# Optimization experiments

Hardware: AMD Instinct MI355X
Metric: run time of the kernel (lower is better)

Reference implementation:

```python
import math
import jax, jax.numpy as jnp
import numpy as np

N_LAYER = 4
D = 256            # n_embd
NH = 4             # n_head
MLP_MULT = 128
VOCAB = 256
N = D * MLP_MULT // NH   # 8192 neurons per head
LN_EPS = 1e-5
TWO_PI = 2.0 * math.pi


def get_freqs(n, theta=2.0 ** 16):
    # quantize(arange(n), q=2) = floor(t/2)*2
    t = jnp.floor(jnp.arange(n, dtype=jnp.float32) / 2.0) * 2.0
    return 1.0 / theta ** (t / n) / TWO_PI


def layernorm(x):
    # nn.LayerNorm(D, elementwise_affine=False): plain normalization
    m = jnp.mean(x, axis=-1, keepdims=True)
    v = jnp.var(x, axis=-1, keepdims=True)
    return (x - m) / jnp.sqrt(v + LN_EPS)


def rope(phases, v):
    # v_rot interleaves (-v_odd, v_even) pairs
    v_rot = jnp.stack((-v[..., 1::2], v[..., ::2]), axis=-1).reshape(v.shape)
    p = (phases % 1.0) * TWO_PI
    return v * jnp.cos(p) + v_rot * jnp.sin(p)


def attention(x_sparse, x):
    # Q = K = x_sparse: (B, nh, T, N); V = x: (B, 1, T, D)
    T = x_sparse.shape[2]
    freqs = get_freqs(N).reshape(1, 1, 1, N)
    phases = jnp.arange(T, dtype=jnp.float32).reshape(1, 1, T, 1) * freqs
    QR = rope(phases, x_sparse)                       # (B, nh, T, N)
    scores = jnp.einsum('bhtn,bhsn->bhts', QR, QR)    # (B, nh, T, T)
    mask = jnp.tril(jnp.ones((T, T), dtype=bool), k=-1)  # strict lower tri
    scores = jnp.where(mask, scores, 0.0)
    return scores @ x                                 # (B, nh, T, D), V broadcast over heads


def bdh_forward(idx, embed, encoder, encoder_v, decoder, lm_head):
    B, T = idx.shape
    x = embed[idx][:, None]        # (B, 1, T, D)
    x = layernorm(x)
    dec = decoder.reshape(NH, N, D)
    for _ in range(N_LAYER):
        x_latent = jnp.einsum('btd,hdn->bhtn', x[:, 0], encoder)   # D -> N expand
        x_sparse = jax.nn.relu(x_latent)
        yKV = attention(x_sparse, x)                               # (B, nh, T, D)
        yKV = layernorm(yKV)
        y_latent = jnp.einsum('bhtd,hdn->bhtn', yKV, encoder_v)
        y_sparse = jax.nn.relu(y_latent)
        xy_sparse = x_sparse * y_sparse                            # gate
        yMLP = jnp.einsum('bhtn,hnd->btd', xy_sparse, dec)         # N -> D decode
        x = layernorm(x + yMLP[:, None])                           # residual + LN
    logits = x[:, 0] @ lm_head    # (B, T, vocab)
    return logits


def setup_inputs() -> dict:
    key = jax.random.key(0)
    k1, k2, k3, k4, k5, k6 = jax.random.split(key, 6)
    B, T = 2, 512
    std = 0.02
    return {
        'idx': jax.random.randint(k1, (B, T), 0, VOCAB, dtype=jnp.int64 if jax.config.jax_enable_x64 else jnp.int32),
        'embed': jax.random.normal(k2, (VOCAB, D), dtype=jnp.float32) * std,
        'encoder': jax.random.normal(k3, (NH, D, N), dtype=jnp.float32) * std,
        'encoder_v': jax.random.normal(k4, (NH, D, N), dtype=jnp.float32) * std,
        'decoder': jax.random.normal(k5, (NH * N, D), dtype=jnp.float32) * std,
        'lm_head': jax.random.normal(k6, (D, VOCAB), dtype=jnp.float32) * std,
    }


def reference(idx, embed, encoder, encoder_v, decoder, lm_head):
    return bdh_forward(idx, embed, encoder, encoder_v, decoder, lm_head)
```

## Files before the change

kernel.cpp:

```cpp
#include <hip/hip_runtime.h>
#include <hip/hip_bf16.h>
#include <cstdio>

#define DEV static __device__ __forceinline__

typedef __attribute__((ext_vector_type(4))) float floatx4;
typedef __attribute__((ext_vector_type(8))) __bf16 bf16x8;

constexpr int Bv = 2, Tv = 512, Dv = 256, NHv = 4, Nv = 8192, NLv = 4, Vv = 256;
constexpr int BTv = Bv * Tv;
constexpr int BHv = Bv * NHv;
constexpr float LNEPS = 1e-5f;
constexpr int KS_SC = 8;
constexpr int KS_DEC = 8;

DEV float b2f(short s) {
    unsigned u = ((unsigned)(unsigned short)s) << 16;
    return __builtin_bit_cast(float, u);
}
DEV short f2b(float f) {
    unsigned u = __builtin_bit_cast(unsigned, f);
    u = (u + 0x7fffu + ((u >> 16) & 1u)) >> 16;
    return (short)u;
}

typedef __attribute__((address_space(3))) unsigned int lds_u32;
typedef const __attribute__((address_space(1))) unsigned int glb_u32;
DEV void gload16(const short* g, short* ldsbase) {
    __builtin_amdgcn_global_load_lds((glb_u32*)g, (lds_u32*)ldsbase, 16, 0, 0);
}

__global__ __launch_bounds__(256) void k_cvtT(const float* __restrict__ in,
                                              short* __restrict__ out, int R, int C) {
    __shared__ float tile[32][33];
    const float* ib = in + (size_t)blockIdx.z * R * C;
    short* ob = out + (size_t)blockIdx.z * R * C;
    int c0 = blockIdx.x * 32, r0 = blockIdx.y * 32;
    int tx = threadIdx.x & 31, ty = threadIdx.x >> 5;
#pragma unroll
    for (int i = 0; i < 4; i++) {
        int r = r0 + ty + i * 8;
        tile[ty + i * 8][tx] = ib[(size_t)r * C + c0 + tx];
    }
    __syncthreads();
#pragma unroll
    for (int i = 0; i < 4; i++) {
        int c = c0 + ty + i * 8;
        ob[(size_t)c * R + r0 + tx] = f2b(tile[tx][ty + i * 8]);
    }
}

__global__ __launch_bounds__(256) void k_transp(const short* __restrict__ xb,
                                                short* __restrict__ xbT) {
    __shared__ short tile[32][33];
    int b = blockIdx.z;
    int t0 = blockIdx.x * 32, d0 = blockIdx.y * 32;
    int tx = threadIdx.x & 31, ty = threadIdx.x >> 5;
#pragma unroll
    for (int i = 0; i < 4; i++)
        tile[ty + i * 8][tx] = xb[((size_t)b * Tv + t0 + ty + i * 8) * Dv + d0 + tx];
    __syncthreads();
#pragma unroll
    for (int i = 0; i < 4; i++)
        xbT[((size_t)b * Dv + d0 + ty + i * 8) * Tv + t0 + tx] = tile[tx][ty + i * 8];
}

__global__ __launch_bounds__(256) void k_rope(unsigned* __restrict__ tab) {
    int i = blockIdx.x * 256 + threadIdx.x;
    int t = blockIdx.y;
    float f = exp2f(-(float)i / 256.0f) * 0.15915494309189535f;
    float ph = fmodf((float)t * f, 1.0f) * 6.2831853071795864f;
    unsigned c = (unsigned short)f2b(cosf(ph));
    unsigned s = (unsigned short)f2b(sinf(ph));
    tab[(size_t)t * (Nv / 2) + i] = c | (s << 16);
}

DEV void reduce2(float& s1, float& s2) {
    __shared__ float r1[4];
    __shared__ float r2[4];
#pragma unroll
    for (int o = 32; o > 0; o >>= 1) {
        s1 += __shfl_down(s1, o, 64);
        s2 += __shfl_down(s2, o, 64);
    }
    int lane = threadIdx.x & 63, w = threadIdx.x >> 6;
    if (lane == 0) { r1[w] = s1; r2[w] = s2; }
    __syncthreads();
    s1 = r1[0] + r1[1] + r1[2] + r1[3];
    s2 = r2[0] + r2[1] + r2[2] + r2[3];
}

DEV float ln_val(float v, float s1, float s2) {
    float m = s1 * (1.0f / Dv);
    float var = s2 * (1.0f / Dv) - m * m;
    float inv = rsqrtf(var + LNEPS);
    return (v - m) * inv;
}

__global__ __launch_bounds__(256) void k_embed_ln(const int* __restrict__ idx,
                                                  const float* __restrict__ embed,
                                                  float* __restrict__ xf, short* __restrict__ xb) {
    int r = blockIdx.x, d = threadIdx.x;
    float v = embed[(size_t)idx[r] * Dv + d];
    float s1 = v, s2 = v * v;
    reduce2(s1, s2);
    float o = ln_val(v, s1, s2);
    xf[(size_t)r * Dv + d] = o;
    xb[(size_t)r * Dv + d] = f2b(o);
}

__global__ __launch_bounds__(256) void k_ln(const float* __restrict__ in,
                                            short* __restrict__ outb) {
    int r = blockIdx.x, d = threadIdx.x;
    size_t o = (size_t)r * Dv + d;
    float v = in[o];
    float s1 = v, s2 = v * v;
    reduce2(s1, s2);
    outb[o] = f2b(ln_val(v, s1, s2));
}

__global__ __launch_bounds__(256) void k_lnsum(const short* __restrict__ ymb,
                                               float* __restrict__ xf, short* __restrict__ xb) {
    int r = blockIdx.x, d = threadIdx.x;
    size_t o = (size_t)r * Dv + d;
    float v = xf[o];
#pragma unroll
    for (int z = 0; z < NHv * KS_DEC; z++)
        v += b2f(ymb[(size_t)z * BTv * Dv + o]);
    float s1 = v, s2 = v * v;
    reduce2(s1, s2);
    float res = ln_val(v, s1, s2);
    xf[o] = res;
    xb[o] = f2b(res);
}

DEV void gemm_main(const short* __restrict__ Ab, int lda,
                   const short* __restrict__ Bb, int ldb, int K,
                   short* sA, short* sB, floatx4 acc[4][4]) {
    const int tid = threadIdx.x;
    const int lane = tid & 63, w = tid >> 6;
    const int wr = w >> 1, wc = w & 1;
    const int lrow = lane & 15;
    const int q = lane >> 4;
    const int rsw = (lrow >> 1) & 3;
    const int srow = lane >> 2;
    const int ssw = (lane & 3) ^ ((lane >> 3) & 3);
    for (int kk = 0; kk < K; kk += 32) {
        __syncthreads();
#pragma unroll
        for (int g2 = 0; g2 < 2; g2++) {
            int brow = g2 * 64 + w * 16;
            int grow = brow + srow;
            gload16(&Ab[(size_t)grow * lda + kk + ssw * 8], &sA[brow * 32]);
            gload16(&Bb[(size_t)grow * ldb + kk + ssw * 8], &sB[brow * 32]);
        }
        __syncthreads();
        bf16x8 aF[4], bF[4];
#pragma unroll
        for (int m = 0; m < 4; m++)
            aF[m] = *(const bf16x8*)&sA[(wr * 64 + m * 16 + lrow) * 32 + ((q ^ rsw) * 8)];
#pragma unroll
        for (int n = 0; n < 4; n++)
            bF[n] = *(const bf16x8*)&sB[(wc * 64 + n * 16 + lrow) * 32 + ((q ^ rsw) * 8)];
#pragma unroll
        for (int m = 0; m < 4; m++)
#pragma unroll
            for (int n = 0; n < 4; n++)
                acc[m][n] = __builtin_amdgcn_mfma_f32_16x16x32_bf16(aF[m], bF[n], acc[m][n], 0, 0, 0);
    }
}

__global__ __launch_bounds__(256) void k_latent(const short* __restrict__ xb,
                                                const short* __restrict__ encT,
                                                const unsigned* __restrict__ ropeT,
                                                short* __restrict__ qr) {
    __shared__ short sA[128 * 32];
    __shared__ short sB[128 * 32];
    int bid = blockIdx.x;
    int xcd = bid & 7, rr = bid >> 3;
    int cmb = xcd + 8 * (rr & 31);
    int mb = rr >> 5;
    int nb = cmb & 63, h = cmb >> 6;
    const short* Ab = xb + (size_t)mb * 128 * Dv;
    const short* Bb = encT + (size_t)h * Nv * Dv + (size_t)nb * 128 * Dv;
    floatx4 acc[4][4] = {};
    gemm_main(Ab, Dv, Bb, Dv, Dv, sA, sB, acc);
    int lane = threadIdx.x & 63, w = threadIdx.x >> 6, wr = w >> 1, wc = w & 1;
    int rb = (lane >> 4) * 4, cb = lane & 15;
    float sgn = (cb & 1) ? 1.0f : -1.0f;
#pragma unroll
    for (int m = 0; m < 4; m++)
#pragma unroll
        for (int n = 0; n < 4; n++) {
            int col = nb * 128 + wc * 64 + n * 16 + cb;
#pragma unroll
            for (int r = 0; r < 4; r++) {
                int row = mb * 128 + wr * 64 + m * 16 + rb + r;
                int b = row >> 9, t = row & 511;
                float v = acc[m][n][r];
                v = v > 0.f ? v : 0.f;
                float vp = __shfl_xor(v, 1);
                unsigned cs = ropeT[(size_t)t * (Nv / 2) + (col >> 1)];
                float c = b2f((short)(cs & 0xffff)), s = b2f((short)(cs >> 16));
                qr[((size_t)(b * NHv + h) * Tv + t) * Nv + col] = f2b(v * c + sgn * vp * s);
            }
        }
}

__global__ __launch_bounds__(256) void k_scores(const short* __restrict__ qr,
                                                short* __restrict__ scs) {
    __shared__ short sA[128 * 32];
    __shared__ short sB[128 * 32];
    int bid = blockIdx.x;
    int xcd = bid & 7, rr = bid >> 3;
    int cmb = xcd + 8 * (rr & 7);
    int pb = rr >> 3;
    int bh = cmb & 7, ks = cmb >> 3;
    int tb = 0;
    while (((tb + 1) * (tb + 2)) / 2 <= pb) tb++;
    int sb = pb - (tb * (tb + 1)) / 2;
    const bool diag = (tb == sb);
    const int KC = Nv / KS_SC;
    const short* Ab = qr + ((size_t)bh * Tv + tb * 128) * Nv + ks * KC;
    const short* Bb = qr + ((size_t)bh * Tv + sb * 128) * Nv + ks * KC;
    floatx4 acc[4][4] = {};
    const int tid = threadIdx.x, lane = tid & 63, w = tid >> 6;
    const int wr = w >> 1, wc = w & 1;
    const int lrow = lane & 15;
    const int q = lane >> 4;
    const int rsw = (lrow >> 1) & 3;
    const int srow = lane >> 2;
    const int ssw = (lane & 3) ^ ((lane >> 3) & 3);
    for (int kk = 0; kk < KC; kk += 32) {
        __syncthreads();
#pragma unroll
        for (int g2 = 0; g2 < 2; g2++) {
            int brow = g2 * 64 + w * 16;
            int grow = brow + srow;
            gload16(&Ab[(size_t)grow * Nv + kk + ssw * 8], &sA[brow * 32]);
            if (!diag)
                gload16(&Bb[(size_t)grow * Nv + kk + ssw * 8], &sB[brow * 32]);
        }
        __syncthreads();
        const short* sBr = diag ? sA : sB;
        bf16x8 aF[4], bF[4];
#pragma unroll
        for (int m = 0; m < 4; m++)
            aF[m] = *(const bf16x8*)&sA[(wr * 64 + m * 16 + lrow) * 32 + ((q ^ rsw) * 8)];
#pragma unroll
        for (int n = 0; n < 4; n++)
            bF[n] = *(const bf16x8*)&sBr[(wc * 64 + n * 16 + lrow) * 32 + ((q ^ rsw) * 8)];
#pragma unroll
        for (int m = 0; m < 4; m++)
#pragma unroll
            for (int n = 0; n < 4; n++)
                acc[m][n] = __builtin_amdgcn_mfma_f32_16x16x32_bf16(aF[m], bF[n], acc[m][n], 0, 0, 0);
    }
    short* slab = scs + ((size_t)ks * BHv + bh) * Tv * Tv;
    int rb = (lane >> 4) * 4, cb = lane & 15;
#pragma unroll
    for (int m = 0; m < 4; m++)
#pragma unroll
        for (int n = 0; n < 4; n++)
#pragma unroll
            for (int r = 0; r < 4; r++) {
                int t = tb * 128 + wr * 64 + m * 16 + rb + r;
                int s = sb * 128 + wc * 64 + n * 16 + cb;
                slab[(size_t)t * Tv + s] = f2b(acc[m][n][r]);
            }
}

__global__ __launch_bounds__(256) void k_redsc(const short* __restrict__ scs,
                                               short* __restrict__ scb) {
    int c = blockIdx.x * 256 + threadIdx.x;
    int row = c >> 6;
    int s0 = (c & 63) * 8;
    int t = row & (Tv - 1);
    float a[8] = {};
#pragma unroll
    for (int ks = 0; ks < KS_SC; ks++) {
        int4 raw = *(const int4*)&scs[((size_t)ks * BHv * Tv + row) * Tv + s0];
        const short* rs = (const short*)&raw;
#pragma unroll
        for (int j = 0; j < 8; j++) a[j] += b2f(rs[j]);
    }
    union { short s[8]; int4 v; } u;
#pragma unroll
    for (int j = 0; j < 8; j++) u.s[j] = (s0 + j < t) ? f2b(a[j]) : 0;
    *(int4*)&scb[(size_t)row * Tv + s0] = u.v;
}

__global__ __launch_bounds__(256) void k_pvg(const short* __restrict__ scb,
                                             const short* __restrict__ xbT,
                                             float* __restrict__ ykv) {
    __shared__ short sA[128 * 32];
    __shared__ short sB[128 * 32];
    int mb = blockIdx.x, nb = blockIdx.y, bh = blockIdx.z;
    int b = bh >> 2;
    const short* Ab = scb + ((size_t)bh * Tv + mb * 128) * Tv;
    const short* Bb = xbT + ((size_t)b * Dv + nb * 128) * Tv;
    floatx4 acc[4][4] = {};
    gemm_main(Ab, Tv, Bb, Tv, (mb + 1) * 128, sA, sB, acc);
    int lane = threadIdx.x & 63, w = threadIdx.x >> 6, wr = w >> 1, wc = w & 1;
    int rb = (lane >> 4) * 4, cb = lane & 15;
#pragma unroll
    for (int m = 0; m < 4; m++)
#pragma unroll
        for (int n = 0; n < 4; n++)
#pragma unroll
            for (int r = 0; r < 4; r++) {
                int t = mb * 128 + wr * 64 + m * 16 + rb + r;
                int d = nb * 128 + wc * 64 + n * 16 + cb;
                ykv[((size_t)bh * Tv + t) * Dv + d] = acc[m][n][r];
            }
}

__global__ __launch_bounds__(256) void k_gate(const short* __restrict__ ykvb,
                                              const short* __restrict__ encvT,
                                              const short* __restrict__ qr,
                                              const unsigned* __restrict__ ropeT,
                                              short* __restrict__ xy) {
    __shared__ short sA[128 * 32];
    __shared__ short sB[128 * 32];
    int bid = blockIdx.x;
    int xcd = bid & 7, rr = bid >> 3;
    int cmb = xcd + 8 * (rr & 31);
    int wi = rr >> 5;
    int mb = wi & 3, bq = wi >> 2;
    int nb = cmb & 63, h = cmb >> 6;
    int bh = bq * NHv + h;
    const short* Ab = ykvb + ((size_t)bh * Tv + mb * 128) * Dv;
    const short* Bb = encvT + (size_t)h * Nv * Dv + (size_t)nb * 128 * Dv;
    floatx4 acc[4][4] = {};
    gemm_main(Ab, Dv, Bb, Dv, Dv, sA, sB, acc);
    int lane = threadIdx.x & 63, w = threadIdx.x >> 6, wr = w >> 1, wc = w & 1;
    int rb = (lane >> 4) * 4, cb = lane & 15;
    int par = cb & 1;
    float sgn = par ? 1.0f : -1.0f;
#pragma unroll
    for (int m = 0; m < 4; m++)
#pragma unroll
        for (int n = 0; n < 4; n++) {
            int col = nb * 128 + wc * 64 + n * 16 + cb;
#pragma unroll
            for (int r = 0; r < 4; r++) {
                int t = mb * 128 + wr * 64 + m * 16 + rb + r;
                size_t idx = ((size_t)bh * Tv + t) * Nv + col;
                unsigned pq = *(const unsigned*)&qr[idx & ~(size_t)1];
                float qlo = b2f((short)(pq & 0xffff)), qhi2 = b2f((short)(pq >> 16));
                float qv = par ? qhi2 : qlo;
                float qp = par ? qlo : qhi2;
                unsigned cs = ropeT[(size_t)t * (Nv / 2) + (col >> 1)];
                float c = b2f((short)(cs & 0xffff)), s = b2f((short)(cs >> 16));
                float xsr = qv * c - sgn * qp * s;
                float v = acc[m][n][r];
                v = v > 0.f ? v : 0.f;
                xy[idx] = f2b(v * xsr);
            }
        }
}

__global__ __launch_bounds__(256) void k_decode(const short* __restrict__ xy,
                                                const short* __restrict__ decT,
                                                short* __restrict__ ymb) {
    __shared__ short sA[128 * 32];
    __shared__ short sB[128 * 32];
    int bid = blockIdx.x;
    int xcd = bid & 7, rr = bid >> 3;
    int cmb = xcd + 8 * (rr & 7);
    int mb = rr >> 3;
    int nb = cmb & 1, h = (cmb >> 1) & 3, ks = cmb >> 3;
    const int KC = Nv / KS_DEC;
    int row0 = mb * 128;
    int b = row0 >> 9, t0 = row0 & 511;
    const short* Ab = xy + ((size_t)(b * NHv + h) * Tv + t0) * Nv + ks * KC;
    const short* Bb = decT + (size_t)h * Dv * Nv + (size_t)nb * 128 * Nv + ks * KC;
    floatx4 acc[4][4] = {};
    gemm_main(Ab, Nv, Bb, Nv, KC, sA, sB, acc);
    short* slab = ymb + (size_t)(h * KS_DEC + ks) * BTv * Dv;
    int lane = threadIdx.x & 63, w = threadIdx.x >> 6, wr = w >> 1, wc = w & 1;
    int rb = (lane >> 4) * 4, cb = lane & 15;
#pragma unroll
    for (int m = 0; m < 4; m++)
#pragma unroll
        for (int n = 0; n < 4; n++)
#pragma unroll
            for (int r = 0; r < 4; r++) {
                int row = row0 + wr * 64 + m * 16 + rb + r;
                int col = nb * 128 + wc * 64 + n * 16 + cb;
                slab[(size_t)row * Dv + col] = f2b(acc[m][n][r]);
            }
}

__global__ __launch_bounds__(256) void k_head(const short* __restrict__ xb,
                                              const short* __restrict__ lmhT,
                                              float* __restrict__ out) {
    __shared__ short sA[128 * 32];
    __shared__ short sB[128 * 32];
    int mb = blockIdx.x, nb = blockIdx.y;
    const short* Ab = xb + (size_t)mb * 128 * Dv;
    const short* Bb = lmhT + (size_t)nb * 128 * Dv;
    floatx4 acc[4][4] = {};
    gemm_main(Ab, Dv, Bb, Dv, Dv, sA, sB, acc);
    int lane = threadIdx.x & 63, w = threadIdx.x >> 6, wr = w >> 1, wc = w & 1;
    int rb = (lane >> 4) * 4, cb = lane & 15;
#pragma unroll
    for (int m = 0; m < 4; m++)
#pragma unroll
        for (int n = 0; n < 4; n++)
#pragma unroll
            for (int r = 0; r < 4; r++) {
                int row = mb * 128 + wr * 64 + m * 16 + rb + r;
                int col = nb * 128 + wc * 64 + n * 16 + cb;
                out[(size_t)row * Vv + col] = acc[m][n][r];
            }
}

extern "C" void kernel_launch(void* const* d_in, const int* in_sizes, int n_in,
                              void* d_out, int out_size, void* d_ws, size_t ws_size,
                              hipStream_t stream) {
    const int* idx = (const int*)d_in[0];
    const float* embed = (const float*)d_in[1];
    const float* enc = (const float*)d_in[2];
    const float* encv = (const float*)d_in[3];
    const float* dec = (const float*)d_in[4];
    const float* lmh = (const float*)d_in[5];
    float* out = (float*)d_out;

    char* w = (char*)d_ws;
    size_t off = 0;
    auto alloc = [&](size_t bytes) -> void* {
        void* p = w + off;
        off = (off + bytes + 255) & ~(size_t)255;
        return p;
    };
    short* encT = (short*)alloc((size_t)NHv * Nv * Dv * 2);
    short* encvT = (short*)alloc((size_t)NHv * Nv * Dv * 2);
    short* decT = (short*)alloc((size_t)NHv * Dv * Nv * 2);
    short* lmhT = (short*)alloc((size_t)Vv * Dv * 2);
    unsigned* ropeT = (unsigned*)alloc((size_t)Tv * (Nv / 2) * 4);
    float* xf = (float*)alloc((size_t)BTv * Dv * 4);
    short* xb = (short*)alloc((size_t)BTv * Dv * 2);
    short* xbT = (short*)alloc((size_t)BTv * Dv * 2);
    short* xy = (short*)alloc((size_t)BHv * Tv * Nv * 2);
    short* qr = (short*)alloc((size_t)BHv * Tv * Nv * 2);
    short* scs = (short*)alloc((size_t)KS_SC * BHv * Tv * Tv * 2);
    short* scb = (short*)alloc((size_t)BHv * Tv * Tv * 2);
    float* ykvf = (float*)alloc((size_t)BHv * Tv * Dv * 4);
    short* ykvb = (short*)alloc((size_t)BHv * Tv * Dv * 2);
    short* ymb = (short*)alloc((size_t)NHv * KS_DEC * BTv * Dv * 2);
    if (off > ws_size) {
        fprintf(stderr, "BDH: workspace too small: need %zu, have %zu\n", off, ws_size);
        return;
    }

    k_cvtT<<<dim3(Nv / 32, Dv / 32, NHv), 256, 0, stream>>>(enc, encT, Dv, Nv);
    k_cvtT<<<dim3(Nv / 32, Dv / 32, NHv), 256, 0, stream>>>(encv, encvT, Dv, Nv);
    k_cvtT<<<dim3(Dv / 32, Nv / 32, NHv), 256, 0, stream>>>(dec, decT, Nv, Dv);
    k_cvtT<<<dim3(Vv / 32, Dv / 32, 1), 256, 0, stream>>>(lmh, lmhT, Dv, Vv);
    k_rope<<<dim3(Nv / 2 / 256, Tv), 256, 0, stream>>>(ropeT);
    k_embed_ln<<<BTv, 256, 0, stream>>>(idx, embed, xf, xb);

    for (int L = 0; L < NLv; L++) {
        k_latent<<<2048, 256, 0, stream>>>(xb, encT, ropeT, qr);
        k_transp<<<dim3(Tv / 32, Dv / 32, Bv), 256, 0, stream>>>(xb, xbT);
        k_scores<<<640, 256, 0, stream>>>(qr, scs);
        k_redsc<<<(BHv * Tv * Tv / 8) / 256, 256, 0, stream>>>(scs, scb);
        k_pvg<<<dim3(Tv / 128, Dv / 128, BHv), 256, 0, stream>>>(scb, xbT, ykvf);
        k_ln<<<BHv * Tv, 256, 0, stream>>>(ykvf, ykvb);
        k_gate<<<2048, 256, 0, stream>>>(ykvb, encvT, qr, ropeT, xy);
        k_decode<<<512, 256, 0, stream>>>(xy, decT, ymb);
        k_lnsum<<<BTv, 256, 0, stream>>>(ymb, xf, xb);
    }
    k_head<<<dim3(BTv / 128, Vv / 128), 256, 0, stream>>>(xb, lmhT, out);
}
```

Before: 765.4 us.

## Double-buffer LDS tiles in GEMM main loops to overlap loads with MFMA

Converts the shared GEMM loop and the scores kernel loop to a two-stage LDS ping-pong. The next K-tile's global-to-LDS loads are issued before the MFMAs on the current tile, with a single waitcnt plus barrier per iteration instead of two syncthreads. This is meant to hide global memory latency behind matrix math. In exchange, LDS per block doubles to 32 KB, which may reduce occupancy.

Result: slower. 936.2 us (+22.3%).

```diff
diff --git a/kernel.cpp b/kernel.cpp
--- a/kernel.cpp
+++ b/kernel.cpp
@@ -13,6 +13,7 @@
 constexpr float LNEPS = 1e-5f;
 constexpr int KS_SC = 8;
 constexpr int KS_DEC = 8;
+constexpr int TILE = 128 * 32;
 
 DEV float b2f(short s) {
     unsigned u = ((unsigned)(unsigned short)s) << 16;
@@ -145,28 +146,42 @@
     const int rsw = (lrow >> 1) & 3;
     const int srow = lane >> 2;
     const int ssw = (lane & 3) ^ ((lane >> 3) & 3);
-    for (int kk = 0; kk < K; kk += 32) {
-        __syncthreads();
-#pragma unroll
-        for (int g2 = 0; g2 < 2; g2++) {
-            int brow = g2 * 64 + w * 16;
-            int grow = brow + srow;
-            gload16(&Ab[(size_t)grow * lda + kk + ssw * 8], &sA[brow * 32]);
-            gload16(&Bb[(size_t)grow * ldb + kk + ssw * 8], &sB[brow * 32]);
+    const int nt = K >> 5;
+#pragma unroll
+    for (int g2 = 0; g2 < 2; g2++) {
+        int brow = g2 * 64 + w * 16;
+        int grow = brow + srow;
+        gload16(&Ab[(size_t)grow * lda + ssw * 8], &sA[brow * 32]);
+        gload16(&Bb[(size_t)grow * ldb + ssw * 8], &sB[brow * 32]);
+    }
+    asm volatile("s_waitcnt vmcnt(0)" ::: "memory");
+    __builtin_amdgcn_s_barrier();
+    for (int t = 0; t < nt; t++) {
+        const int cur = (t & 1) * TILE, nxt = ((t + 1) & 1) * TILE;
+        if (t + 1 < nt) {
+            int kk = (t + 1) * 32;
+#pragma unroll
+            for (int g2 = 0; g2 < 2; g2++) {
+                int brow = g2 * 64 + w * 16;
+                int grow = brow + srow;
+                gload16(&Ab[(size_t)grow * lda + kk + ssw * 8], &sA[nxt + brow * 32]);
+                gload16(&Bb[(size_t)grow * ldb + kk + ssw * 8], &sB[nxt + brow * 32]);
+            }
         }
-        __syncthreads();
         bf16x8 aF[4], bF[4];
 #pragma unroll
         for (int m = 0; m < 4; m++)
-            aF[m] = *(const bf16x8*)&sA[(wr * 64 + m * 16 + lrow) * 32 + ((q ^ rsw) * 8)];
+            aF[m] = *(const bf16x8*)&sA[cur + (wr * 64 + m * 16 + lrow) * 32 + ((q ^ rsw) * 8)];
 #pragma unroll
         for (int n = 0; n < 4; n++)
-            bF[n] = *(const bf16x8*)&sB[(wc * 64 + n * 16 + lrow) * 32 + ((q ^ rsw) * 8)];
+            bF[n] = *(const bf16x8*)&sB[cur + (wc * 64 + n * 16 + lrow) * 32 + ((q ^ rsw) * 8)];
 #pragma unroll
         for (int m = 0; m < 4; m++)
 #pragma unroll
             for (int n = 0; n < 4; n++)
                 acc[m][n] = __builtin_amdgcn_mfma_f32_16x16x32_bf16(aF[m], bF[n], acc[m][n], 0, 0, 0);
+        asm volatile("s_waitcnt vmcnt(0) lgkmcnt(0)" ::: "memory");
+        __builtin_amdgcn_s_barrier();
     }
 }
 
@@ -174,8 +189,8 @@
                                                 const short* __restrict__ encT,
                                                 const unsigned* __restrict__ ropeT,
                                                 short* __restrict__ qr) {
-    __shared__ short sA[128 * 32];
-    __shared__ short sB[128 * 32];
+    __shared__ short sA[2 * TILE];
+    __shared__ short sB[2 * TILE];
     int bid = blockIdx.x;
     int xcd = bid & 7, rr = bid >> 3;
     int cmb = xcd + 8 * (rr & 31);
@@ -209,8 +224,8 @@
 
 __global__ __launch_bounds__(256) void k_scores(const short* __restrict__ qr,
                                                 short* __restrict__ scs) {
-    __shared__ short sA[128 * 32];
-    __shared__ short sB[128 * 32];
+    __shared__ short sA[2 * TILE];
+    __shared__ short sB[2 * TILE];
     int bid = blockIdx.x;
     int xcd = bid & 7, rr = bid >> 3;
     int cmb = xcd + 8 * (rr & 7);
@@ -231,30 +246,43 @@
     const int rsw = (lrow >> 1) & 3;
     const int srow = lane >> 2;
     const int ssw = (lane & 3) ^ ((lane >> 3) & 3);
-    for (int kk = 0; kk < KC; kk += 32) {
-        __syncthreads();
-#pragma unroll
-        for (int g2 = 0; g2 < 2; g2++) {
-            int brow = g2 * 64 + w * 16;
-            int grow = brow + srow;
-            gload16(&Ab[(size_t)grow * Nv + kk + ssw * 8], &sA[brow * 32]);
-            if (!diag)
-                gload16(&Bb[(size_t)grow * Nv + kk + ssw * 8], &sB[brow * 32]);
+    const int nt = KC >> 5;
+#pragma unroll
+    for (int g2 = 0; g2 < 2; g2++) {
+        int brow = g2 * 64 + w * 16;
+        int grow = brow + srow;
+        gload16(&Ab[(size_t)grow * Nv + ssw * 8], &sA[brow * 32]);
+        if (!diag) gload16(&Bb[(size_t)grow * Nv + ssw * 8], &sB[brow * 32]);
+    }
+    asm volatile("s_waitcnt vmcnt(0)" ::: "memory");
+    __builtin_amdgcn_s_barrier();
+    for (int t = 0; t < nt; t++) {
+        const int cur = (t & 1) * TILE, nxt = ((t + 1) & 1) * TILE;
+        if (t + 1 < nt) {
+            int kk = (t + 1) * 32;
+#pragma unroll
+            for (int g2 = 0; g2 < 2; g2++) {
+                int brow = g2 * 64 + w * 16;
+                int grow = brow + srow;
+                gload16(&Ab[(size_t)grow * Nv + kk + ssw * 8], &sA[nxt + brow * 32]);
+                if (!diag) gload16(&Bb[(size_t)grow * Nv + kk + ssw * 8], &sB[nxt + brow * 32]);
+            }
         }
-        __syncthreads();
         const short* sBr = diag ? sA : sB;
         bf16x8 aF[4], bF[4];
 #pragma unroll
         for (int m = 0; m < 4; m++)
-            aF[m] = *(const bf16x8*)&sA[(wr * 64 + m * 16 + lrow) * 32 + ((q ^ rsw) * 8)];
+            aF[m] = *(const bf16x8*)&sA[cur + (wr * 64 + m * 16 + lrow) * 32 + ((q ^ rsw) * 8)];
 #pragma unroll
         for (int n = 0; n < 4; n++)
-            bF[n] = *(const bf16x8*)&sBr[(wc * 64 + n * 16 + lrow) * 32 + ((q ^ rsw) * 8)];
+            bF[n] = *(const bf16x8*)&sBr[cur + (wc * 64 + n * 16 + lrow) * 32 + ((q ^ rsw) * 8)];
 #pragma unroll
         for (int m = 0; m < 4; m++)
 #pragma unroll
             for (int n = 0; n < 4; n++)
                 acc[m][n] = __builtin_amdgcn_mfma_f32_16x16x32_bf16(aF[m], bF[n], acc[m][n], 0, 0, 0);
+        asm volatile("s_waitcnt vmcnt(0) lgkmcnt(0)" ::: "memory");
+        __builtin_amdgcn_s_barrier();
     }
     short* slab = scs + ((size_t)ks * BHv + bh) * Tv * Tv;
     int rb = (lane >> 4) * 4, cb = lane & 15;
@@ -293,8 +321,8 @@
 __global__ __launch_bounds__(256) void k_pvg(const short* __restrict__ scb,
                                              const short* __restrict__ xbT,
                                              float* __restrict__ ykv) {
-    __shared__ short sA[128 * 32];
-    __shared__ short sB[128 * 32];
+    __shared__ short sA[2 * TILE];
+    __shared__ short sB[2 * TILE];
     int mb = blockIdx.x, nb = blockIdx.y, bh = blockIdx.z;
     int b = bh >> 2;
     const short* Ab = scb + ((size_t)bh * Tv + mb * 128) * Tv;
@@ -320,8 +348,8 @@
                                               const short* __restrict__ qr,
                                               const unsigned* __restrict__ ropeT,
                                               short* __restrict__ xy) {
-    __shared__ short sA[128 * 32];
-    __shared__ short sB[128 * 32];
+    __shared__ short sA[2 * TILE];
+    __shared__ short sB[2 * TILE];
     int bid = blockIdx.x;
     int xcd = bid & 7, rr = bid >> 3;
     int cmb = xcd + 8 * (rr & 31);
@@ -363,8 +391,8 @@
 __global__ __launch_bounds__(256) void k_decode(const short* __restrict__ xy,
                                                 const short* __restrict__ decT,
                                                 short* __restrict__ ymb) {
-    __shared__ short sA[128 * 32];
-    __shared__ short sB[128 * 32];
+    __shared__ short sA[2 * TILE];
+    __shared__ short sB[2 * TILE];
     int bid = blockIdx.x;
     int xcd = bid & 7, rr = bid >> 3;
     int cmb = xcd + 8 * (rr & 7);
@@ -395,8 +423,8 @@
 __global__ __launch_bounds__(256) void k_head(const short* __restrict__ xb,
                                               const short* __restrict__ lmhT,
                                               float* __restrict__ out) {
-    __shared__ short sA[128 * 32];
-    __shared__ short sB[128 * 32];
+    __shared__ short sA[2 * TILE];
+    __shared__ short sB[2 * TILE];
     int mb = blockIdx.x, nb = blockIdx.y;
     const short* Ab = xb + (size_t)mb * 128 * Dv;
     const short* Bb = lmhT + (size_t)nb * 128 * Dv;
```
